# Performance work log

Hardware: AMD Instinct MI355X
Metric: run time of the kernel (lower is better)

Reference implementation:

```python
import jax, jax.numpy as jnp
import numpy as np

NEG = -9e15

def _gat_layer(x, adj, W, a_src, a_dst):
    # x: [B,N,Fin], W: [Fin,Fout], a_src/a_dst: [Fout], adj: [N,N]
    h = jnp.einsum('bnf,fo->bno', x, W)                    # [B,N,Fout]
    e_src = jnp.einsum('bno,o->bn', h, a_src)              # [B,N]
    e_dst = jnp.einsum('bno,o->bn', h, a_dst)              # [B,N]
    e = jax.nn.leaky_relu(e_src[:, :, None] + e_dst[:, None, :], 0.2)  # [B,N,N]
    att = jax.nn.softmax(jnp.where(adj > 0, e, NEG), axis=-1)
    return jnp.einsum('bij,bjo->bio', att, h)              # [B,N,Fout]

def setup_inputs() -> dict:
    key = jax.random.key(0)
    ks = jax.random.split(key, 12)
    B, N, Fin = 8, 2048, 128
    H = [128, 128, 64]
    C = 128
    s = lambda *d: 1.0 / np.sqrt(d[0])
    inp = {
        'x':   jax.random.normal(ks[0], (B, N, Fin), jnp.float32),
        'adj': jax.random.normal(ks[1], (N, N), jnp.float32),
        'W1':  jax.random.normal(ks[2], (Fin, H[0]), jnp.float32) * s(Fin),
        'a1s': jax.random.normal(ks[3], (H[0],), jnp.float32) * s(H[0]),
        'a1d': jax.random.normal(ks[4], (H[0],), jnp.float32) * s(H[0]),
        'W2':  jax.random.normal(ks[5], (H[0], H[1]), jnp.float32) * s(H[0]),
        'a2s': jax.random.normal(ks[6], (H[1],), jnp.float32) * s(H[1]),
        'a2d': jax.random.normal(ks[7], (H[1],), jnp.float32) * s(H[1]),
        'W3':  jax.random.normal(ks[8], (H[1], H[2]), jnp.float32) * s(H[1]),
        'a3s': jax.random.normal(ks[9], (H[2],), jnp.float32) * s(H[2]),
        'a3d': jax.random.normal(ks[10], (H[2],), jnp.float32) * s(H[2]),
        'Wlin': jax.random.normal(ks[11], (H[2] * N, C), jnp.float32) * s(H[2] * N),
        'blin': jnp.zeros((C,), jnp.float32),
    }
    return inp

def reference(x, adj, W1, a1s, a1d, W2, a2s, a2d, W3, a3s, a3d, Wlin, blin):
    out = jax.nn.relu(_gat_layer(x, adj, W1, a1s, a1d))
    out = jax.nn.relu(_gat_layer(out, adj, W2, a2s, a2d))
    out = jax.nn.relu(_gat_layer(out, adj, W3, a3s, a3d))
    B = out.shape[0]
    out = out.reshape(B, -1)              # flatten [B, N*H3]
    return out @ Wlin + blin              # [B, num_classes]
```

## Files before the change

kernel.cpp:

```cpp
#include <hip/hip_runtime.h>
#include <stdint.h>


typedef unsigned short u16;
typedef __bf16 bf16x8 __attribute__((ext_vector_type(8)));
typedef float f32x4 __attribute__((ext_vector_type(4)));
typedef u16 u16x8 __attribute__((ext_vector_type(8)));

#define LOG2E 1.44269504088896340736f

__device__ __forceinline__ float b2f(u16 u) {
    union { unsigned int i; float f; } v; v.i = ((unsigned int)u) << 16; return v.f;
}
__device__ __forceinline__ u16 f2b(float f) {
    union { float f; unsigned int i; } v; v.f = f;
    unsigned int i = v.i;
    return (u16)((i + 0x7fffu + ((i >> 16) & 1u)) >> 16);
}
__device__ __forceinline__ float fast_exp2(float x) {
#if __has_builtin(__builtin_amdgcn_exp2f)
    return __builtin_amdgcn_exp2f(x);
#else
    return exp2f(x);
#endif
}

union ABfrag { bf16x8 v; u16x8 u; };

__device__ __forceinline__ void gload_lds16(const u16* g, u16* l) {
    __builtin_amdgcn_global_load_lds((const __attribute__((address_space(1))) void*)g,
                                     (__attribute__((address_space(3))) void*)l,
                                     16, 0, 0);
}

__global__ void __launch_bounds__(256) k_mask(const float* __restrict__ adj,
                                              uint32_t* __restrict__ adjm) {
    const int w = threadIdx.x >> 6, lane = threadIdx.x & 63;
    const int row = blockIdx.x * 4 + w;
    const float* ar = adj + (size_t)row * 2048;
    uint32_t* mr = adjm + (size_t)row * 64;
    for (int j0 = 0; j0 < 2048; j0 += 64) {
        unsigned long long m = __ballot(ar[j0 + lane] > 0.f);
        if (lane == 0) {
            mr[(j0 >> 5)] = (uint32_t)m;
            mr[(j0 >> 5) + 1] = (uint32_t)(m >> 32);
        }
    }
}

__global__ void k_prep(const float* __restrict__ W1, const float* __restrict__ W2,
                       const float* __restrict__ W3,
                       const float* __restrict__ a1s, const float* __restrict__ a1d,
                       const float* __restrict__ a2s, const float* __restrict__ a2d,
                       const float* __restrict__ a3s, const float* __restrict__ a3d,
                       u16* __restrict__ Wt1, u16* __restrict__ Wt2, u16* __restrict__ Wt3,
                       float* __restrict__ u1s, float* __restrict__ u1d,
                       float* __restrict__ u2s, float* __restrict__ u2d,
                       float* __restrict__ u3s, float* __restrict__ u3d) {
    if (blockIdx.x == 160) {
        int f = threadIdx.x;
        if (f < 128) {
            float s1 = 0.f, d1 = 0.f, s2 = 0.f, d2 = 0.f, s3 = 0.f, d3 = 0.f;
            for (int o = 0; o < 128; ++o) { float w = W1[f * 128 + o]; s1 += w * a1s[o]; d1 += w * a1d[o]; }
            for (int o = 0; o < 128; ++o) { float w = W2[f * 128 + o]; s2 += w * a2s[o]; d2 += w * a2d[o]; }
            for (int o = 0; o <  64; ++o) { float w = W3[f *  64 + o]; s3 += w * a3s[o]; d3 += w * a3d[o]; }
            u1s[f] = s1 * LOG2E; u1d[f] = d1 * LOG2E;
            u2s[f] = s2 * LOG2E; u2d[f] = d2 * LOG2E;
            u3s[f] = s3 * LOG2E; u3d[f] = d3 * LOG2E;
        }
        return;
    }
    int idx = blockIdx.x * 256 + threadIdx.x;
    if (idx < 16384) {
        int f = idx >> 7, o = idx & 127;
        Wt1[o * 128 + f] = f2b(W1[idx]);
    } else if (idx < 32768) {
        int j = idx - 16384; int f = j >> 7, o = j & 127;
        Wt2[o * 128 + f] = f2b(W2[j]);
    } else if (idx < 40960) {
        int j = idx - 32768; int f = j >> 6, o = j & 63;
        Wt3[o * 128 + f] = f2b(W3[j]);
    }
}

template <int F, bool XF32>
__global__ void __launch_bounds__(256) k_h(const void* __restrict__ xv,
                                           const u16* __restrict__ Wt,
                                           const float* __restrict__ us,
                                           const float* __restrict__ ud,
                                           u16* __restrict__ h_t,
                                           float* __restrict__ esf,
                                           float* __restrict__ edf) {
    constexpr int NT = F / 16;
    constexpr int TNP = 72;
    __shared__ __align__(16) u16 hl[F * TNP];

    const int b = blockIdx.x;
    const int nblk = blockIdx.y;
    const int tid = threadIdx.x;
    const int w = tid >> 6, lane = tid & 63;
    const int quad = lane >> 4, l15 = lane & 15;
    const int n0w = nblk * 64 + w * 16;
    const int i_a = n0w + l15;

    ABfrag afr[4];
    float ps = 0.f, pd = 0.f;
    if (XF32) {
        const float* xr = (const float*)xv + ((size_t)(b * 2048 + i_a)) * 128;
#pragma unroll
        for (int kk = 0; kk < 4; ++kk) {
            const int o8 = kk * 32 + quad * 8;
            float4 x0 = *reinterpret_cast<const float4*>(xr + o8);
            float4 x1 = *reinterpret_cast<const float4*>(xr + o8 + 4);
            float4 s0 = *reinterpret_cast<const float4*>(us + o8);
            float4 s1 = *reinterpret_cast<const float4*>(us + o8 + 4);
            float4 d0 = *reinterpret_cast<const float4*>(ud + o8);
            float4 d1 = *reinterpret_cast<const float4*>(ud + o8 + 4);
            ps += x0.x * s0.x + x0.y * s0.y + x0.z * s0.z + x0.w * s0.w
                + x1.x * s1.x + x1.y * s1.y + x1.z * s1.z + x1.w * s1.w;
            pd += x0.x * d0.x + x0.y * d0.y + x0.z * d0.z + x0.w * d0.w
                + x1.x * d1.x + x1.y * d1.y + x1.z * d1.z + x1.w * d1.w;
            afr[kk].u[0] = f2b(x0.x); afr[kk].u[1] = f2b(x0.y);
            afr[kk].u[2] = f2b(x0.z); afr[kk].u[3] = f2b(x0.w);
            afr[kk].u[4] = f2b(x1.x); afr[kk].u[5] = f2b(x1.y);
            afr[kk].u[6] = f2b(x1.z); afr[kk].u[7] = f2b(x1.w);
        }
    } else {
        const u16* xr = (const u16*)xv + ((size_t)(b * 2048 + i_a)) * 128;
#pragma unroll
        for (int kk = 0; kk < 4; ++kk) {
            const int o8 = kk * 32 + quad * 8;
            u16x8 xa = *reinterpret_cast<const u16x8*>(xr + o8);
            afr[kk].u = xa;
            float4 s0 = *reinterpret_cast<const float4*>(us + o8);
            float4 s1 = *reinterpret_cast<const float4*>(us + o8 + 4);
            float4 d0 = *reinterpret_cast<const float4*>(ud + o8);
            float4 d1 = *reinterpret_cast<const float4*>(ud + o8 + 4);
            float xf[8];
#pragma unroll
            for (int j = 0; j < 8; ++j) xf[j] = b2f(xa[j]);
            ps += xf[0] * s0.x + xf[1] * s0.y + xf[2] * s0.z + xf[3] * s0.w
                + xf[4] * s1.x + xf[5] * s1.y + xf[6] * s1.z + xf[7] * s1.w;
            pd += xf[0] * d0.x + xf[1] * d0.y + xf[2] * d0.z + xf[3] * d0.w
                + xf[4] * d1.x + xf[5] * d1.y + xf[6] * d1.z + xf[7] * d1.w;
        }
    }
    ps += __shfl_xor(ps, 16, 64); ps += __shfl_xor(ps, 32, 64);
    pd += __shfl_xor(pd, 16, 64); pd += __shfl_xor(pd, 32, 64);
    if (quad == 0) {
        const size_t idx = (size_t)(b * 2048 + i_a) * 2;
        float2 sv; sv.x = fast_exp2(ps); sv.y = fast_exp2(0.2f * ps);
        float2 dv; dv.x = fast_exp2(pd); dv.y = fast_exp2(0.2f * pd);
        *reinterpret_cast<float2*>(esf + idx) = sv;
        *reinterpret_cast<float2*>(edf + idx) = dv;
    }

    f32x4 acc[NT];
#pragma unroll
    for (int nt = 0; nt < NT; ++nt) acc[nt] = (f32x4){0.f, 0.f, 0.f, 0.f};
#pragma unroll
    for (int kk = 0; kk < 4; ++kk) {
#pragma unroll
        for (int nt = 0; nt < NT; ++nt) {
            bf16x8 bfv = *reinterpret_cast<const bf16x8*>(
                Wt + (nt * 16 + l15) * 128 + kk * 32 + quad * 8);
            acc[nt] = __builtin_amdgcn_mfma_f32_16x16x32_bf16(afr[kk].v, bfv, acc[nt], 0, 0, 0);
        }
    }

#pragma unroll
    for (int nt = 0; nt < NT; ++nt)
#pragma unroll
        for (int r = 0; r < 4; ++r)
            hl[(nt * 16 + l15) * TNP + w * 16 + quad * 4 + r] = f2b(acc[nt][r]);
    __syncthreads();
    if (tid < F * 2) {
        int o = tid >> 1, half = tid & 1;
        const u16* src = hl + o * TNP + half * 32;
        u16* dst = h_t + ((size_t)(b * F + o)) * 2048 + nblk * 64 + half * 32;
#pragma unroll
        for (int c = 0; c < 4; ++c)
            *reinterpret_cast<u16x8*>(dst + c * 8) =
                *reinterpret_cast<const u16x8*>(src + c * 8);
    }
}

template <int F, bool OUT_F32>
__global__ void __launch_bounds__(512) k_attn(const float* __restrict__ esf,
                                              const float* __restrict__ edf,
                                              const uint32_t* __restrict__ adjm,
                                              const u16* __restrict__ h_t,
                                              void* __restrict__ outp) {
    constexpr int NT = F / 16;
    __shared__ __align__(16) u16 Ht[2][2][F * 64];
    float* accLDS = (float*)&Ht[0][0][0];

    const int b = blockIdx.x;
    const int iblk = blockIdx.y;
    const int tid = threadIdx.x;
    const int grp = tid >> 8;
    const int t8 = tid & 255;
    const int w = t8 >> 6;
    const int lane = tid & 63;
    const int quad = lane >> 4, l15 = lane & 15;
    const int i_a = iblk * 64 + w * 16 + l15;

    const float2 esp = *reinterpret_cast<const float2*>(esf + ((size_t)(b * 2048 + i_a)) * 2);
    const float Es = esp.x, Fs = esp.y;
    const float* edb = edf + (size_t)b * 4096;
    const uint2* mrow = (const uint2*)(adjm + (size_t)i_a * 64);
    const u16* hb = h_t + (size_t)b * F * 2048;

    const int lro = lane >> 3;
    const int lcp = lane & 7;
    const int jt0 = grp * 16;

    ABfrag onesf;
#pragma unroll
    for (int j = 0; j < 8; ++j) onesf.u[j] = 0x3F80;

    f32x4 acc[NT];
#pragma unroll
    for (int nt = 0; nt < NT; ++nt) acc[nt] = (f32x4){0.f, 0.f, 0.f, 0.f};
    f32x4 dccc = (f32x4){0.f, 0.f, 0.f, 0.f};

    {
        const int j0 = jt0 * 64;
#pragma unroll
        for (int it = 0; it < F / 32; ++it) {
            int ro = (it * 4 + w) * 8 + lro;
            int c = lcp ^ (ro & 7);
            gload_lds16(hb + (size_t)ro * 2048 + j0 + c * 8, &Ht[grp][0][(it * 4 + w) * 512]);
        }
    }
    f32x4 ec[8];
    {
        const float* eb = edb + (size_t)(jt0 * 64 + quad * 8) * 2;
#pragma unroll
        for (int q = 0; q < 4; ++q) ec[q] = *reinterpret_cast<const f32x4*>(eb + q * 4);
#pragma unroll
        for (int q = 0; q < 4; ++q) ec[4 + q] = *reinterpret_cast<const f32x4*>(eb + 64 + q * 4);
    }
    uint2 mc = mrow[jt0];
    __syncthreads();

#pragma unroll 2
    for (int jj = 0; jj < 16; ++jj) {
        const int cur = jj & 1, nxt = cur ^ 1;
        f32x4 en[8]; uint2 mn;
        if (jj < 15) {
            const int j1 = (jt0 + jj + 1) * 64;
#pragma unroll
            for (int it = 0; it < F / 32; ++it) {
                int ro = (it * 4 + w) * 8 + lro;
                int c = lcp ^ (ro & 7);
                gload_lds16(hb + (size_t)ro * 2048 + j1 + c * 8, &Ht[grp][nxt][(it * 4 + w) * 512]);
            }
            const float* eb = edb + (size_t)(j1 + quad * 8) * 2;
#pragma unroll
            for (int q = 0; q < 4; ++q) en[q] = *reinterpret_cast<const f32x4*>(eb + q * 4);
#pragma unroll
            for (int q = 0; q < 4; ++q) en[4 + q] = *reinterpret_cast<const f32x4*>(eb + 64 + q * 4);
            mn = mrow[jt0 + jj + 1];
        }

        ABfrag af[2];
#pragma unroll
        for (int kk = 0; kk < 2; ++kk) {
            const uint32_t word = kk ? mc.y : mc.x;
#pragma unroll
            for (int px = 0; px < 4; ++px) {
                const f32x4 q = ec[kk * 4 + px];
                float w0 = fmaxf(Es * q.x, Fs * q.y);
                float w1 = fmaxf(Es * q.z, Fs * q.w);
                const uint32_t s0 = 0u - ((word >> (quad * 8 + px * 2)) & 1u);
                const uint32_t s1 = 0u - ((word >> (quad * 8 + px * 2 + 1)) & 1u);
                w0 = __uint_as_float(__float_as_uint(w0) & s0);
                w1 = __uint_as_float(__float_as_uint(w1) & s1);
                af[kk].v[px * 2]     = (__bf16)w0;
                af[kk].v[px * 2 + 1] = (__bf16)w1;
            }
        }

#pragma unroll
        for (int kk = 0; kk < 2; ++kk) {
#pragma unroll
            for (int nt = 0; nt < NT; ++nt) {
                int ob = nt * 16 + l15;
                int c = kk * 4 + quad;
                bf16x8 bfv = *reinterpret_cast<const bf16x8*>(
                    &Ht[grp][cur][ob * 64 + ((c ^ (ob & 7)) * 8)]);
                acc[nt] = __builtin_amdgcn_mfma_f32_16x16x32_bf16(af[kk].v, bfv, acc[nt], 0, 0, 0);
            }
            dccc = __builtin_amdgcn_mfma_f32_16x16x32_bf16(af[kk].v, onesf.v, dccc, 0, 0, 0);
        }

        if (jj < 15) {
#pragma unroll
            for (int q = 0; q < 8; ++q) ec[q] = en[q];
            mc = mn;
        }
        __syncthreads();
    }

    if (grp == 1) {
#pragma unroll
        for (int nt = 0; nt < NT; ++nt)
            *reinterpret_cast<f32x4*>(&accLDS[(t8 * (NT + 1) + nt) * 4]) = acc[nt];
        *reinterpret_cast<f32x4*>(&accLDS[(t8 * (NT + 1) + NT) * 4]) = dccc;
    }
    __syncthreads();
    if (grp == 0) {
#pragma unroll
        for (int nt = 0; nt < NT; ++nt)
            acc[nt] += *reinterpret_cast<const f32x4*>(&accLDS[(t8 * (NT + 1) + nt) * 4]);
        dccc += *reinterpret_cast<const f32x4*>(&accLDS[(t8 * (NT + 1) + NT) * 4]);
        float dinv[4];
#pragma unroll
        for (int r = 0; r < 4; ++r)
            dinv[r] = 1.0f / fmaxf(dccc[r], 1e-30f);
        const int ib = iblk * 64 + w * 16 + quad * 4;
        if (OUT_F32) {
            float* o3 = (float*)outp;
#pragma unroll
            for (int nt = 0; nt < NT; ++nt)
#pragma unroll
                for (int r = 0; r < 4; ++r) {
                    float vv = fmaxf(acc[nt][r] * dinv[r], 0.f);
                    o3[((size_t)(b * 2048 + ib + r)) * F + nt * 16 + l15] = vv;
                }
        } else {
            u16* xo = (u16*)outp;
#pragma unroll
            for (int nt = 0; nt < NT; ++nt)
#pragma unroll
                for (int r = 0; r < 4; ++r) {
                    float vv = fmaxf(acc[nt][r] * dinv[r], 0.f);
                    xo[((size_t)(b * 2048 + ib + r)) * F + nt * 16 + l15] = f2b(vv);
                }
        }
    }
}

__global__ void __launch_bounds__(256) k_lin(const float* __restrict__ o3,
                                             const float* __restrict__ Wlin,
                                             float* __restrict__ pbuf) {
    __shared__ float xc[8][256];
    __shared__ float red[8][8][128];
    const int tid = threadIdx.x;
    const int k0 = blockIdx.x * 256;
    for (int idx = tid; idx < 2048; idx += 256) {
        int bb = idx >> 8, kk = idx & 255;
        xc[bb][kk] = o3[(size_t)bb * 131072 + k0 + kk];
    }
    __syncthreads();
    const int o4 = tid & 31;
    const int kb = tid >> 5;
    f32x4 acc[8];
#pragma unroll
    for (int bb = 0; bb < 8; ++bb) acc[bb] = (f32x4){0.f, 0.f, 0.f, 0.f};
    const float* wp = Wlin + (size_t)(k0 + kb * 32) * 128 + o4 * 4;
#pragma unroll 4
    for (int k = 0; k < 32; ++k) {
        f32x4 wv = *reinterpret_cast<const f32x4*>(wp + (size_t)k * 128);
#pragma unroll
        for (int bb = 0; bb < 8; ++bb) acc[bb] += wv * xc[bb][kb * 32 + k];
    }
#pragma unroll
    for (int bb = 0; bb < 8; ++bb)
        *reinterpret_cast<f32x4*>(&red[kb][bb][o4 * 4]) = acc[bb];
    __syncthreads();
    const int f = tid * 4;
    const int bb = f >> 7, o = f & 127;
    f32x4 s = (f32x4){0.f, 0.f, 0.f, 0.f};
#pragma unroll
    for (int k2 = 0; k2 < 8; ++k2) s += *reinterpret_cast<const f32x4*>(&red[k2][bb][o]);
    *reinterpret_cast<f32x4*>(&pbuf[(size_t)blockIdx.x * 1024 + f]) = s;
}

__global__ void __launch_bounds__(256) k_bias(const float* __restrict__ pbuf,
                                              const float* __restrict__ blin,
                                              float* __restrict__ out) {
    __shared__ float red[256];
    const int tid = threadIdx.x;
    const int p16 = tid >> 4;
    const int fo = tid & 15;
    const int f0 = blockIdx.x * 16;
    float s = 0.f;
#pragma unroll 4
    for (int p = p16; p < 512; p += 16)
        s += pbuf[(size_t)p * 1024 + f0 + fo];
    red[tid] = s;
    __syncthreads();
    if (tid < 16) {
        float t = 0.f;
#pragma unroll
        for (int k = 0; k < 16; ++k) t += red[k * 16 + tid];
        out[f0 + tid] = t + blin[(f0 + tid) & 127];
    }
}

extern "C" void kernel_launch(void* const* d_in, const int* in_sizes, int n_in,
                              void* d_out, int out_size, void* d_ws, size_t ws_size,
                              hipStream_t stream) {
    (void)in_sizes; (void)n_in; (void)out_size;
    const float* x    = (const float*)d_in[0];
    const float* adj  = (const float*)d_in[1];
    const float* W1   = (const float*)d_in[2];
    const float* a1s  = (const float*)d_in[3];
    const float* a1d  = (const float*)d_in[4];
    const float* W2   = (const float*)d_in[5];
    const float* a2s  = (const float*)d_in[6];
    const float* a2d  = (const float*)d_in[7];
    const float* W3   = (const float*)d_in[8];
    const float* a3s  = (const float*)d_in[9];
    const float* a3d  = (const float*)d_in[10];
    const float* Wlin = (const float*)d_in[11];
    const float* blin = (const float*)d_in[12];

    char* ws = (char*)d_ws;
    u16*   h_t = (u16*)ws;
    size_t off = (size_t)4 << 20;
    float* esf = (float*)(ws + off); off += 131072;
    float* edf = (float*)(ws + off); off += 131072;
    u16*   Wt1 = (u16*)(ws + off);   off += 32768;
    u16*   Wt2 = (u16*)(ws + off);   off += 32768;
    u16*   Wt3 = (u16*)(ws + off);   off += 16384;
    float* u1s = (float*)(ws + off); off += 512;
    float* u1d = (float*)(ws + off); off += 512;
    float* u2s = (float*)(ws + off); off += 512;
    float* u2d = (float*)(ws + off); off += 512;
    float* u3s = (float*)(ws + off); off += 512;
    float* u3d = (float*)(ws + off); off += 512;
    uint32_t* adjm = (uint32_t*)(ws + off); off += 524288;
    float* pbuf = (float*)(ws + off); off += (size_t)512 * 1024 * 4;
    u16* actA;
    if (ws_size >= off + ((size_t)4 << 20)) {
        actA = (u16*)(ws + off);
    } else {
        actA = (u16*)d_in[0];
    }
    float* o3 = (float*)actA;

    dim3 g(8, 32);
    k_mask<<<512, 256, 0, stream>>>(adj, adjm);
    k_prep<<<161, 256, 0, stream>>>(W1, W2, W3, a1s, a1d, a2s, a2d, a3s, a3d,
                                    Wt1, Wt2, Wt3, u1s, u1d, u2s, u2d, u3s, u3d);

    k_h<128, true ><<<g, 256, 0, stream>>>((const void*)x, Wt1, u1s, u1d, h_t, esf, edf);
    k_attn<128, false><<<g, 512, 0, stream>>>(esf, edf, adjm, h_t, (void*)actA);

    k_h<128, false><<<g, 256, 0, stream>>>((const void*)actA, Wt2, u2s, u2d, h_t, esf, edf);
    k_attn<128, false><<<g, 512, 0, stream>>>(esf, edf, adjm, h_t, (void*)actA);

    k_h<64, false><<<g, 256, 0, stream>>>((const void*)actA, Wt3, u3s, u3d, h_t, esf, edf);
    k_attn<64, true ><<<g, 512, 0, stream>>>(esf, edf, adjm, h_t, (void*)o3);

    k_lin<<<512, 256, 0, stream>>>(o3, Wlin, pbuf);
    k_bias<<<64, 256, 0, stream>>>(pbuf, blin, (float*)d_out);
}
```

Baseline: 264.6 us.

## Triple-buffer attention H tiles and stage edge scores and masks in LDS

The attention kernel moves from a double-buffered to a triple-buffered global-to-LDS pipeline for the H tiles. It uses explicit vmcnt waits and a single barrier per iteration, so loads run two tiles ahead. The dst edge scores and the block's adjacency mask rows are preloaded into LDS (the mask with an XOR swizzle) instead of read from global each step, and MFMA sections get raised wave priority. The extra LDS use (added H slot plus about 32KB for scores and masks) may lower occupancy, and the hand-placed waitcnt and barrier logic is fragile.

Result: faster. 240.4 us (-9.1%).

```diff
diff --git a/kernel.cpp b/kernel.cpp
--- a/kernel.cpp
+++ b/kernel.cpp
@@ -31,6 +31,15 @@
     __builtin_amdgcn_global_load_lds((const __attribute__((address_space(1))) void*)g,
                                      (__attribute__((address_space(3))) void*)l,
                                      16, 0, 0);
+}
+
+template <int N>
+__device__ __forceinline__ void wait_vmcnt() {
+    asm volatile("s_waitcnt vmcnt(%0)" :: "i"(N) : "memory");
+}
+__device__ __forceinline__ void pipe_barrier() {
+    __builtin_amdgcn_s_barrier();
+    asm volatile("" ::: "memory");
 }
 
 __global__ void __launch_bounds__(256) k_mask(const float* __restrict__ adj,
@@ -192,7 +201,10 @@
                                               const u16* __restrict__ h_t,
                                               void* __restrict__ outp) {
     constexpr int NT = F / 16;
-    __shared__ __align__(16) u16 Ht[2][2][F * 64];
+    constexpr int G  = F / 32;
+    __shared__ __align__(16) u16 Ht[2][3][F * 64];
+    __shared__ __align__(16) float eL[4096];
+    __shared__ __align__(16) uint32_t mL[64 * 64];
     float* accLDS = (float*)&Ht[0][0][0];
 
     const int b = blockIdx.x;
@@ -204,11 +216,10 @@
     const int lane = tid & 63;
     const int quad = lane >> 4, l15 = lane & 15;
     const int i_a = iblk * 64 + w * 16 + l15;
+    const int r_loc = w * 16 + l15;
 
     const float2 esp = *reinterpret_cast<const float2*>(esf + ((size_t)(b * 2048 + i_a)) * 2);
     const float Es = esp.x, Fs = esp.y;
-    const float* edb = edf + (size_t)b * 4096;
-    const uint2* mrow = (const uint2*)(adjm + (size_t)i_a * 64);
     const u16* hb = h_t + (size_t)b * F * 2048;
 
     const int lro = lane >> 3;
@@ -225,45 +236,42 @@
     f32x4 dccc = (f32x4){0.f, 0.f, 0.f, 0.f};
 
     {
-        const int j0 = jt0 * 64;
-#pragma unroll
-        for (int it = 0; it < F / 32; ++it) {
+        const float4* esrc = (const float4*)(edf + (size_t)b * 4096);
+        float4* edst = (float4*)eL;
+#pragma unroll
+        for (int t = 0; t < 2; ++t) edst[tid + t * 512] = esrc[tid + t * 512];
+        const uint2* msrc = (const uint2*)(adjm + (size_t)(iblk * 64) * 64);
+#pragma unroll
+        for (int t = 0; t < 4; ++t) {
+            int idx = tid + t * 512;
+            int r = idx >> 5, k = idx & 31;
+            uint2 v = msrc[idx];
+            *reinterpret_cast<uint2*>((char*)mL + r * 256 + ((k ^ (r & 31)) * 8)) = v;
+        }
+    }
+
+    auto STAGE = [&](int jt, int slot) {
+        const int j0 = jt * 64;
+        u16* lbase = &Ht[grp][slot][0];
+#pragma unroll
+        for (int it = 0; it < G; ++it) {
             int ro = (it * 4 + w) * 8 + lro;
             int c = lcp ^ (ro & 7);
-            gload_lds16(hb + (size_t)ro * 2048 + j0 + c * 8, &Ht[grp][0][(it * 4 + w) * 512]);
-        }
-    }
-    f32x4 ec[8];
-    {
-        const float* eb = edb + (size_t)(jt0 * 64 + quad * 8) * 2;
-#pragma unroll
-        for (int q = 0; q < 4; ++q) ec[q] = *reinterpret_cast<const f32x4*>(eb + q * 4);
-#pragma unroll
-        for (int q = 0; q < 4; ++q) ec[4 + q] = *reinterpret_cast<const f32x4*>(eb + 64 + q * 4);
-    }
-    uint2 mc = mrow[jt0];
-    __syncthreads();
-
-#pragma unroll 2
-    for (int jj = 0; jj < 16; ++jj) {
-        const int cur = jj & 1, nxt = cur ^ 1;
-        f32x4 en[8]; uint2 mn;
-        if (jj < 15) {
-            const int j1 = (jt0 + jj + 1) * 64;
-#pragma unroll
-            for (int it = 0; it < F / 32; ++it) {
-                int ro = (it * 4 + w) * 8 + lro;
-                int c = lcp ^ (ro & 7);
-                gload_lds16(hb + (size_t)ro * 2048 + j1 + c * 8, &Ht[grp][nxt][(it * 4 + w) * 512]);
-            }
-            const float* eb = edb + (size_t)(j1 + quad * 8) * 2;
-#pragma unroll
-            for (int q = 0; q < 4; ++q) en[q] = *reinterpret_cast<const f32x4*>(eb + q * 4);
-#pragma unroll
-            for (int q = 0; q < 4; ++q) en[4 + q] = *reinterpret_cast<const f32x4*>(eb + 64 + q * 4);
-            mn = mrow[jt0 + jj + 1];
-        }
-
+            gload_lds16(hb + (size_t)ro * 2048 + j0 + c * 8, lbase + (it * 4 + w) * 512);
+        }
+    };
+
+    f32x4 ec[8]; uint2 mc;
+    auto loadE = [&](int jt, f32x4* e, uint2& m) {
+        const float* eb = eL + (size_t)(jt * 64 + quad * 8) * 2;
+#pragma unroll
+        for (int q = 0; q < 4; ++q) e[q] = *reinterpret_cast<const f32x4*>(eb + q * 4);
+#pragma unroll
+        for (int q = 0; q < 4; ++q) e[4 + q] = *reinterpret_cast<const f32x4*>(eb + 64 + q * 4);
+        m = *reinterpret_cast<const uint2*>((const char*)mL + r_loc * 256 + ((jt ^ (r_loc & 31)) * 8));
+    };
+
+    auto compute = [&](int slot) {
         ABfrag af[2];
 #pragma unroll
         for (int kk = 0; kk < 2; ++kk) {
@@ -281,7 +289,8 @@
                 af[kk].v[px * 2 + 1] = (__bf16)w1;
             }
         }
-
+        const u16* tb = &Ht[grp][slot][0];
+        __builtin_amdgcn_s_setprio(1);
 #pragma unroll
         for (int kk = 0; kk < 2; ++kk) {
 #pragma unroll
@@ -289,20 +298,38 @@
                 int ob = nt * 16 + l15;
                 int c = kk * 4 + quad;
                 bf16x8 bfv = *reinterpret_cast<const bf16x8*>(
-                    &Ht[grp][cur][ob * 64 + ((c ^ (ob & 7)) * 8)]);
+                    tb + ob * 64 + ((c ^ (ob & 7)) * 8));
                 acc[nt] = __builtin_amdgcn_mfma_f32_16x16x32_bf16(af[kk].v, bfv, acc[nt], 0, 0, 0);
             }
             dccc = __builtin_amdgcn_mfma_f32_16x16x32_bf16(af[kk].v, onesf.v, dccc, 0, 0, 0);
         }
-
-        if (jj < 15) {
-#pragma unroll
-            for (int q = 0; q < 8; ++q) ec[q] = en[q];
-            mc = mn;
-        }
-        __syncthreads();
-    }
-
+        __builtin_amdgcn_s_setprio(0);
+    };
+
+    __syncthreads();
+    loadE(jt0, ec, mc);
+    STAGE(jt0, 0);
+    STAGE(jt0 + 1, 1);
+
+    int sc = 0, sp = 2;
+    for (int jj = 0; jj < 15; ++jj) {
+        wait_vmcnt<G>();
+        pipe_barrier();
+        if (jj < 14) STAGE(jt0 + jj + 2, sp);
+        f32x4 en[8]; uint2 mn;
+        loadE(jt0 + jj + 1, en, mn);
+        compute(sc);
+#pragma unroll
+        for (int q = 0; q < 8; ++q) ec[q] = en[q];
+        mc = mn;
+        sc = (sc == 2) ? 0 : sc + 1;
+        sp = (sp == 2) ? 0 : sp + 1;
+    }
+    wait_vmcnt<0>();
+    pipe_barrier();
+    compute(sc);
+
+    __syncthreads();
     if (grp == 1) {
 #pragma unroll
         for (int nt = 0; nt < NT; ++nt)
```
